# Kernel optimization log

Hardware: AMD Instinct MI355X
Metric: run time of the kernel (lower is better)

## Reference

```python
import jax, jax.numpy as jnp
import numpy as np

EPS = 1e-3          # keras BatchNormalization default epsilon
DT = 0.2
LAM2 = 4.0          # lambda_diffusion**2 = 2.0**2
K = 5

def _bn(x, gamma, beta, mean, var):
    # inference-mode batch norm over channel (last) axis
    return (x - mean) * jax.lax.rsqrt(var + EPS) * gamma + beta

def _conv(x, w):
    # NHWC 'same' conv, stride 1, no bias
    return jax.lax.conv_general_dilated(x, w, (1, 1), 'SAME',
                                        dimension_numbers=('NHWC', 'HWIO', 'NHWC'))

def _sobel_edges(x):
    # tf.image.sobel_edges: per-channel 3x3 Sobel with REFLECT padding.
    # returns (dy, dx) matching sobel[...,0], sobel[...,1]
    p = jnp.pad(x, ((0, 0), (1, 1), (1, 1), (0, 0)), mode='reflect')
    dy = (p[:, 2:, :-2] + 2 * p[:, 2:, 1:-1] + p[:, 2:, 2:]) \
       - (p[:, :-2, :-2] + 2 * p[:, :-2, 1:-1] + p[:, :-2, 2:])
    dx = (p[:, :-2, 2:] + 2 * p[:, 1:-1, 2:] + p[:, 2:, 2:]) \
       - (p[:, :-2, :-2] + 2 * p[:, 1:-1, :-2] + p[:, 2:, :-2])
    return dy, dx

def setup_inputs() -> dict:
    key = jax.random.key(0)
    k1, k2, k3 = jax.random.split(key, 3)
    B, H, W, Cin, Cout = 16, 128, 128, 64, 64
    c = jnp.float32
    return {
        'x':   jax.random.normal(k1, (B, H, W, Cin), dtype=c),
        'f_w': jax.random.normal(k2, (3, 3, Cin, Cout), dtype=c) * 0.05,
        'g_w': jax.random.normal(k3, (3, 3, Cout, Cout), dtype=c) * 0.05,
        'bnf_gamma': jnp.ones((Cin,), c),  'bnf_beta': jnp.zeros((Cin,), c),
        'bnf_mean':  jnp.zeros((Cin,), c), 'bnf_var':  jnp.ones((Cin,), c),
        'bng_gamma': jnp.ones((Cout,), c), 'bng_beta': jnp.zeros((Cout,), c),
        'bng_mean':  jnp.zeros((Cout,), c),'bng_var':  jnp.ones((Cout,), c),
        'bno_gamma': jnp.ones((Cout,), c), 'bno_beta': jnp.zeros((Cout,), c),
        'bno_mean':  jnp.zeros((Cout,), c),'bno_var':  jnp.ones((Cout,), c),
    }

def reference(x, f_w, g_w,
              bnf_gamma, bnf_beta, bnf_mean, bnf_var,
              bng_gamma, bng_beta, bng_mean, bng_var,
              bno_gamma, bno_beta, bno_mean, bno_var):
    f = _conv(jax.nn.relu(_bn(x, bnf_gamma, bnf_beta, bnf_mean, bnf_var)), f_w)
    h = f
    g = _conv(jax.nn.relu(_bn(h, bng_gamma, bng_beta, bng_mean, bng_var)), g_w)
    g1 = g
    dy, dx = _sobel_edges(h)
    Dx = 1.0 / (dy * dy / LAM2 + 1.0)   # source: sobel[..., 0]
    Dy = 1.0 / (dx * dx / LAM2 + 1.0)   # source: sobel[..., 1]
    # NOTE: faithful to source — rolls on axis=2 (W) and axis=3 (channels in NHWC)
    ux = 0.5 * (jnp.roll(g, 1, axis=2) - jnp.roll(g, -1, axis=2))
    vy = 0.5 * (jnp.roll(g1, 1, axis=3) - jnp.roll(g1, -1, axis=3))
    Ax = g * DT
    Ay = g1 * DT
    Bx = Dx * DT
    By = Dy * DT
    E = (ux + vy) * DT
    D = 1.0 / (1.0 + 2 * Bx + 2 * By)
    h0 = h
    for _ in range(K):
        prev = h
        h = D * ((1 - 2 * Bx - 2 * By) * h0
                 - 2 * E * h
                 + (-Ax + 2 * Bx) * jnp.roll(h, 1, axis=2)
                 + ( Ax + 2 * Bx) * jnp.roll(h, -1, axis=2)
                 + (-Ay + 2 * By) * jnp.roll(h, 1, axis=3)
                 + ( Ay + 2 * By) * jnp.roll(h, -1, axis=3)
                 + 2 * DT * f)
        h0 = prev
    h = jax.nn.relu(_bn(h, bno_gamma, bno_beta, bno_mean, bno_var))
    return (h, g)
```

## Files before the change

### kernel.cpp

```cpp
#include <hip/hip_runtime.h>

#define HH 128
#define WW 128
#define CC 64
#define ROW (WW*CC)
#define SLOTB 128
#define ROWB (130*SLOTB)
#define FSTR 68

typedef _Float16 half8 __attribute__((ext_vector_type(8)));
typedef _Float16 half4v __attribute__((ext_vector_type(4)));
typedef float floatx4 __attribute__((ext_vector_type(4)));

__device__ inline floatx4 rcp4(floatx4 v)
{
    floatx4 r;
    r[0] = __builtin_amdgcn_rcpf(v[0]);
    r[1] = __builtin_amdgcn_rcpf(v[1]);
    r[2] = __builtin_amdgcn_rcpf(v[2]);
    r[3] = __builtin_amdgcn_rcpf(v[3]);
    return r;
}

__global__ __launch_bounds__(256)
void repack_w(const float* __restrict__ wf, const float* __restrict__ wg,
              _Float16* __restrict__ W2f, _Float16* __restrict__ W2g)
{
    int idx = blockIdx.x * 256 + threadIdx.x;
    int sel = idx >= 36864;
    int id  = sel ? idx - 36864 : idx;
    const float* src = sel ? wg : wf;
    _Float16* dst = sel ? W2g : W2f;
    int t = id >> 12, c = (id >> 6) & 63, o = id & 63;
    int kc = c >> 5, q = (c >> 3) & 3, j = c & 7;
    int pos = ((((t*2 + kc)*4 + q)*64 + o) << 3) + j;
    dst[pos] = (_Float16)src[id];
}

template<int BNIN, int EPI>
__global__ __launch_bounds__(256, 2)
void conv_mfma(const void* __restrict__ srcv, const _Float16* __restrict__ W2,
               _Float16* __restrict__ outH, float* __restrict__ outF,
               _Float16* __restrict__ y2,
               const float* __restrict__ ig, const float* __restrict__ ib,
               const float* __restrict__ imu, const float* __restrict__ iva,
               const float* __restrict__ og, const float* __restrict__ ob,
               const float* __restrict__ om, const float* __restrict__ ov)
{
    __shared__ __align__(16) char smem[69632];
    const int t = threadIdx.x;
    const int blk = ((blockIdx.x & 7) << 7) | (blockIdx.x >> 3);
    const int b = blk >> 6, i0 = (blk & 63) * 2;

    const int c8 = (t & 7) << 3;
    float scv[8], biv[8];
    if (BNIN) {
        #pragma unroll
        for (int j = 0; j < 8; ++j) {
            float s = ig[c8+j] * rsqrtf(iva[c8+j] + 1e-3f);
            scv[j] = s; biv[j] = ib[c8+j] - imu[c8+j]*s;
        }
    }

    {
        int rr = t >> 6, s = (t >> 5) & 1;
        *(float*)(smem + rr*ROWB + (s ? 129*SLOTB : 0) + ((t & 31) << 2)) = 0.f;
    }

    if (BNIN) {
        for (int r = 0; r < 4; ++r) {
            int iy = i0 - 1 + r;
            bool inb = (iy >= 0) && (iy < HH);
            #pragma unroll
            for (int k = 0; k < 4; ++k) {
                int idx = t + (k << 8);
                int px = idx >> 3;
                half8 v = {0,0,0,0,0,0,0,0};
                if (inb) {
                    const float* gp = (const float*)srcv
                        + ((size_t)(b*HH + iy))*ROW + px*CC + c8;
                    float4 u0 = *(const float4*)gp;
                    float4 u1 = *(const float4*)(gp + 4);
                    v[0] = (_Float16)fmaxf(0.f, u0.x*scv[0] + biv[0]);
                    v[1] = (_Float16)fmaxf(0.f, u0.y*scv[1] + biv[1]);
                    v[2] = (_Float16)fmaxf(0.f, u0.z*scv[2] + biv[2]);
                    v[3] = (_Float16)fmaxf(0.f, u0.w*scv[3] + biv[3]);
                    v[4] = (_Float16)fmaxf(0.f, u1.x*scv[4] + biv[4]);
                    v[5] = (_Float16)fmaxf(0.f, u1.y*scv[5] + biv[5]);
                    v[6] = (_Float16)fmaxf(0.f, u1.z*scv[6] + biv[6]);
                    v[7] = (_Float16)fmaxf(0.f, u1.w*scv[7] + biv[7]);
                }
                int key = ((px + 1) & 7) << 4;
                *(half8*)(smem + r*ROWB + (px + 1)*SLOTB
                          + ((((t & 7) << 4)) ^ key)) = v;
            }
        }
    } else {
        const _Float16* src = (const _Float16*)srcv;
        #pragma unroll
        for (int r = 0; r < 4; ++r) {
            int iy = i0 - 1 + r;
            char* lb = smem + r*ROWB + SLOTB;
            if (iy >= 0 && iy < HH) {
                const _Float16* gp = src + (size_t)(b*HH + iy)*ROW;
                #pragma unroll
                for (int k = 0; k < 4; ++k) {
                    int eo = ((k << 8) + t) << 3;
                    __builtin_amdgcn_global_load_lds(
                        (const __attribute__((address_space(1))) void*)(gp + eo),
                        (__attribute__((address_space(3))) void*)(lb + (eo << 1)),
                        16, 0, 0);
                }
            } else {
                half8 z = {0,0,0,0,0,0,0,0};
                #pragma unroll
                for (int k = 0; k < 4; ++k)
                    *(half8*)(lb + (((k << 8) + t) << 4)) = z;
            }
        }
    }
    __syncthreads();

    const int wv = t >> 6, lane = t & 63;
    const int lm = lane & 15, quad = lane >> 4;
    const int r  = wv >> 1;
    const int px0 = (wv & 1) * 64;
    floatx4 z4 = {0.f,0.f,0.f,0.f};
    floatx4 acc[4][4];
    #pragma unroll
    for (int ms = 0; ms < 4; ++ms)
        #pragma unroll
        for (int nt = 0; nt < 4; ++nt) acc[ms][nt] = z4;

    #pragma unroll
    for (int tap = 0; tap < 9; ++tap) {
        const int di = tap / 3, dj = tap % 3;
        const int slot = px0 + lm + dj;
        const int key  = (slot & 7) << 4;
        const char* abase = smem + (r + di)*ROWB + slot*SLOTB;
        #pragma unroll
        for (int kc = 0; kc < 2; ++kc) {
            const char* ab = abase + ((kc*64 + quad*16) ^ key);
            half8 a0 = *(const half8*)(ab);
            half8 a1 = *(const half8*)(ab + 16*SLOTB);
            half8 a2 = *(const half8*)(ab + 32*SLOTB);
            half8 a3 = *(const half8*)(ab + 48*SLOTB);
            const _Float16* wb = W2 + (((tap*2 + kc)*4 + quad) << 9) + (lm << 3);
            half8 b0 = *(const half8*)(wb);
            half8 b1 = *(const half8*)(wb + 128);
            half8 b2 = *(const half8*)(wb + 256);
            half8 b3 = *(const half8*)(wb + 384);
            acc[0][0] = __builtin_amdgcn_mfma_f32_16x16x32_f16(a0, b0, acc[0][0], 0,0,0);
            acc[1][0] = __builtin_amdgcn_mfma_f32_16x16x32_f16(a1, b0, acc[1][0], 0,0,0);
            acc[2][0] = __builtin_amdgcn_mfma_f32_16x16x32_f16(a2, b0, acc[2][0], 0,0,0);
            acc[3][0] = __builtin_amdgcn_mfma_f32_16x16x32_f16(a3, b0, acc[3][0], 0,0,0);
            acc[0][1] = __builtin_amdgcn_mfma_f32_16x16x32_f16(a0, b1, acc[0][1], 0,0,0);
            acc[1][1] = __builtin_amdgcn_mfma_f32_16x16x32_f16(a1, b1, acc[1][1], 0,0,0);
            acc[2][1] = __builtin_amdgcn_mfma_f32_16x16x32_f16(a2, b1, acc[2][1], 0,0,0);
            acc[3][1] = __builtin_amdgcn_mfma_f32_16x16x32_f16(a3, b1, acc[3][1], 0,0,0);
            acc[0][2] = __builtin_amdgcn_mfma_f32_16x16x32_f16(a0, b2, acc[0][2], 0,0,0);
            acc[1][2] = __builtin_amdgcn_mfma_f32_16x16x32_f16(a1, b2, acc[1][2], 0,0,0);
            acc[2][2] = __builtin_amdgcn_mfma_f32_16x16x32_f16(a2, b2, acc[2][2], 0,0,0);
            acc[3][2] = __builtin_amdgcn_mfma_f32_16x16x32_f16(a3, b2, acc[3][2], 0,0,0);
            acc[0][3] = __builtin_amdgcn_mfma_f32_16x16x32_f16(a0, b3, acc[0][3], 0,0,0);
            acc[1][3] = __builtin_amdgcn_mfma_f32_16x16x32_f16(a1, b3, acc[1][3], 0,0,0);
            acc[2][3] = __builtin_amdgcn_mfma_f32_16x16x32_f16(a2, b3, acc[2][3], 0,0,0);
            acc[3][3] = __builtin_amdgcn_mfma_f32_16x16x32_f16(a3, b3, acc[3][3], 0,0,0);
        }
    }

    __syncthreads();
    float* sF = (float*)smem;
    #pragma unroll
    for (int nt = 0; nt < 4; ++nt) {
        int c = nt*16 + lm;
        #pragma unroll
        for (int ms = 0; ms < 4; ++ms) {
            int pix = r*128 + px0 + ms*16 + quad*4;
            floatx4 v = acc[ms][nt];
            #pragma unroll
            for (int rv = 0; rv < 4; ++rv)
                sF[(pix + rv)*FSTR + c] = v[rv];
        }
    }
    __syncthreads();

    const size_t gbase = ((size_t)(b*HH + i0)) * ROW;
    if (EPI) {
        const int c8o = (t & 7) << 3;
        float s8[8], bb8[8];
        #pragma unroll
        for (int j = 0; j < 8; ++j) {
            float ss = og[c8o+j] * rsqrtf(ov[c8o+j] + 1e-3f);
            s8[j] = ss; bb8[j] = ob[c8o+j] - om[c8o+j]*ss;
        }
        #pragma unroll
        for (int jj = 0; jj < 8; ++jj) {
            int chunk = jj*256 + t;
            int px = chunk >> 3;
            const float* sp = sF + px*FSTR + c8o;
            floatx4 u0 = *(const floatx4*)(sp);
            floatx4 u1 = *(const floatx4*)(sp + 4);
            half8 hv, yv;
            #pragma unroll
            for (int j = 0; j < 4; ++j) {
                hv[j]   = (_Float16)u0[j];
                hv[4+j] = (_Float16)u1[j];
                yv[j]   = (_Float16)fmaxf(0.f, u0[j]*s8[j]   + bb8[j]);
                yv[4+j] = (_Float16)fmaxf(0.f, u1[j]*s8[4+j] + bb8[4+j]);
            }
            size_t oe = gbase + (size_t)px*64 + c8o;
            *(half8*)(outH + oe) = hv;
            int key8 = ((px + 1) & 7) << 3;
            *(half8*)(y2 + gbase + (size_t)px*64 + (c8o ^ key8)) = yv;
        }
    } else {
        #pragma unroll
        for (int jj = 0; jj < 8; ++jj) {
            int chunk = jj*256 + t;
            int px = chunk >> 3;
            const int cc = (t & 7) << 3;
            const float* sp = sF + px*FSTR + cc;
            size_t oe = gbase + (size_t)px*64 + cc;
            *(floatx4*)(outF + oe)     = *(const floatx4*)(sp);
            *(floatx4*)(outF + oe + 4) = *(const floatx4*)(sp + 4);
        }
    }
}

__global__ __launch_bounds__(1024, 2)
void diffuse(const _Float16* __restrict__ f, const float* __restrict__ g,
             float* __restrict__ out,
             const float* __restrict__ bog, const float* __restrict__ bob,
             const float* __restrict__ bom, const float* __restrict__ bov)
{
    __shared__ float B0[ROW], B1[ROW];
    const int t = threadIdx.x;
    const int rowb = ((blockIdx.x & 7) << 8) | (blockIdx.x >> 3);
    const int b = rowb >> 7, i = rowb & 127;
    const int im = (i == 0)    ? 1    : i - 1;
    const int ip = (i == HH-1) ? HH-2 : i + 1;
    const _Float16* fb  = f + (size_t)b * (HH*ROW);
    const _Float16* frm = fb + (size_t)im * ROW;
    const _Float16* fr0 = fb + (size_t)i  * ROW;
    const _Float16* frp = fb + (size_t)ip * ROW;
    const float* grow = g + (size_t)rowb * ROW;

    const int lane = t & 63;
    const int srcm = (lane & 48) | ((lane - 1) & 15);
    const int srcp = (lane & 48) | ((lane + 1) & 15);
    const int w0 = t >> 4, c0 = (t & 15) << 2;
    const int qch[2] = { t*4, t*4 + 4096 };
    const int wch[2] = { w0, w0 + 64 };

    #pragma unroll
    for (int k = 0; k < 2; ++k) {
        half4v vm = *(const half4v*)(frm + qch[k]);
        half4v vp = *(const half4v*)(frp + qch[k]);
        floatx4 a = { (float)vm[0], (float)vm[1], (float)vm[2], (float)vm[3] };
        floatx4 p = { (float)vp[0], (float)vp[1], (float)vp[2], (float)vp[3] };
        *(floatx4*)(B0 + qch[k]) = a;
        *(floatx4*)(B1 + qch[k]) = p;
    }
    __syncthreads();

    floatx4 Bx4[2], dxp4[2];
    #pragma unroll
    for (int k = 0; k < 2; ++k) {
        int w = wch[k];
        int wm = (w == 0)    ? 1      : w - 1;
        int wp = (w == WW-1) ? WW - 2 : w + 1;
        floatx4 am = *(const floatx4*)(B0 + wm*CC + c0);
        floatx4 a0 = *(const floatx4*)(B0 + w *CC + c0);
        floatx4 ap = *(const floatx4*)(B0 + wp*CC + c0);
        floatx4 bm = *(const floatx4*)(B1 + wm*CC + c0);
        floatx4 b0 = *(const floatx4*)(B1 + w *CC + c0);
        floatx4 bp = *(const floatx4*)(B1 + wp*CC + c0);
        floatx4 dy = (bm + 2.f*b0 + bp) - (am + 2.f*a0 + ap);
        Bx4[k]  = 0.2f * rcp4(dy*dy*0.25f + 1.f);
        dxp4[k] = (ap - am) + (bp - bm);
    }
    __syncthreads();

    #pragma unroll
    for (int k = 0; k < 2; ++k) {
        half4v v0 = *(const half4v*)(fr0 + qch[k]);
        floatx4 fv = { (float)v0[0], (float)v0[1], (float)v0[2], (float)v0[3] };
        *(floatx4*)(B0 + qch[k]) = fv;
        *(floatx4*)(B1 + qch[k]) = *(const floatx4*)(grow + qch[k]);
    }
    __syncthreads();

    floatx4 cR4[2], cL4[2], cU4[2], cH0[2], cEE[2], cF[2], h4[2], h04[2];
    #pragma unroll
    for (int k = 0; k < 2; ++k) {
        int w = wch[k];
        int wm = (w == 0)    ? 1      : w - 1;
        int wp = (w == WW-1) ? WW - 2 : w + 1;
        int wl = (w + WW - 1) & (WW - 1);
        int wr = (w + 1) & (WW - 1);
        floatx4 fm = *(const floatx4*)(B0 + wm*CC + c0);
        floatx4 fv = *(const floatx4*)(B0 + w *CC + c0);
        floatx4 fp = *(const floatx4*)(B0 + wp*CC + c0);
        floatx4 dx = dxp4[k] + 2.f*(fp - fm);
        floatx4 By = 0.2f * rcp4(dx*dx*0.25f + 1.f);
        floatx4 Bx = Bx4[k];
        floatx4 gv = *(const floatx4*)(B1 + w *CC + c0);
        floatx4 gl = *(const floatx4*)(B1 + wl*CC + c0);
        floatx4 gr = *(const floatx4*)(B1 + wr*CC + c0);
        float gdm = __shfl(gv[3], srcm, 64);
        float gup = __shfl(gv[0], srcp, 64);
        floatx4 gd = { gdm, gv[0], gv[1], gv[2] };
        floatx4 gu = { gv[1], gv[2], gv[3], gup };
        floatx4 E  = ((gl - gr) + (gd - gu)) * 0.1f;
        floatx4 Dd = rcp4(1.f + 2.f*Bx + 2.f*By);
        floatx4 P  = 2.f * Bx * Dd;
        floatx4 R  = 2.f * By * Dd;
        floatx4 Q  = (gv * 0.2f) * Dd;
        cR4[k] = P + Q;
        cL4[k] = P - Q;
        cU4[k] = R + Q;
        cH0[k] = 2.f*Dd - 1.f;
        cEE[k] = -2.f * E * Dd;
        cF[k]  = 0.4f * Dd * fv;
        h4[k] = fv; h04[k] = fv;
    }
    __syncthreads();

    int oWl[2], oWr[2];
    #pragma unroll
    for (int k = 0; k < 2; ++k) {
        int w = wch[k];
        oWl[k] = ((w + WW - 1) & (WW - 1))*CC + c0;
        oWr[k] = ((w + 1) & (WW - 1))*CC + c0;
    }

    float* cur = B0;
    float* oth = B1;
    for (int it = 0; it < 5; ++it) {
        #pragma unroll
        for (int k = 0; k < 2; ++k) {
            floatx4 hl = *(const floatx4*)(cur + oWl[k]);
            floatx4 hr = *(const floatx4*)(cur + oWr[k]);
            floatx4 hv = h4[k];
            float hdm = __shfl(hv[3], srcm, 64);
            float hup = __shfl(hv[0], srcp, 64);
            floatx4 hd = { hdm, hv[0], hv[1], hv[2] };
            floatx4 hu = { hv[1], hv[2], hv[3], hup };
            floatx4 cD = (cU4[k] - cR4[k]) + cL4[k];
            floatx4 hn = cH0[k]*h04[k] + cEE[k]*hv
                       + cR4[k]*hr + cL4[k]*hl
                       + cU4[k]*hu + cD*hd + cF[k];
            if (it < 4)
                *(floatx4*)(oth + qch[k]) = hn;
            h04[k] = hv; h4[k] = hn;
        }
        if (it < 4) {
            __syncthreads();
            float* tmp = cur; cur = oth; oth = tmp;
        }
    }

    floatx4 gg = *(const floatx4*)(bog + c0);
    floatx4 vv = *(const floatx4*)(bov + c0);
    floatx4 bb = *(const floatx4*)(bob + c0);
    floatx4 mm = *(const floatx4*)(bom + c0);
    floatx4 s4, bi4;
    #pragma unroll
    for (int j = 0; j < 4; ++j) s4[j] = gg[j] * rsqrtf(vv[j] + 1e-3f);
    bi4 = bb - mm*s4;
    float* op = out + (size_t)rowb * ROW;
    #pragma unroll
    for (int k = 0; k < 2; ++k) {
        floatx4 rr = h4[k]*s4 + bi4;
        #pragma unroll
        for (int j = 0; j < 4; ++j) rr[j] = fmaxf(0.f, rr[j]);
        *(floatx4*)(op + qch[k]) = rr;
    }
}

extern "C" void kernel_launch(void* const* d_in, const int* in_sizes, int n_in,
                              void* d_out, int out_size, void* d_ws, size_t ws_size,
                              hipStream_t stream)
{
    const float* x    = (const float*)d_in[0];
    const float* f_w  = (const float*)d_in[1];
    const float* g_w  = (const float*)d_in[2];
    const float* bnf_g = (const float*)d_in[3];
    const float* bnf_b = (const float*)d_in[4];
    const float* bnf_m = (const float*)d_in[5];
    const float* bnf_v = (const float*)d_in[6];
    const float* bng_g = (const float*)d_in[7];
    const float* bng_b = (const float*)d_in[8];
    const float* bng_m = (const float*)d_in[9];
    const float* bng_v = (const float*)d_in[10];
    const float* bno_g = (const float*)d_in[11];
    const float* bno_b = (const float*)d_in[12];
    const float* bno_m = (const float*)d_in[13];
    const float* bno_v = (const float*)d_in[14];

    float* out = (float*)d_out;
    const size_t N = (size_t)16 * HH * WW * CC;
    _Float16* y2   = (_Float16*)d_ws;
    _Float16* fbuf = y2 + N;
    _Float16* W2f  = y2 + 2*N;
    _Float16* W2g  = W2f + 36864;

    repack_w<<<288, 256, 0, stream>>>(f_w, g_w, W2f, W2g);
    conv_mfma<1,1><<<1024, 256, 0, stream>>>(x, W2f, fbuf, nullptr, y2,
                                             bnf_g, bnf_b, bnf_m, bnf_v,
                                             bng_g, bng_b, bng_m, bng_v);
    conv_mfma<0,0><<<1024, 256, 0, stream>>>(y2, W2g, nullptr, out + N, nullptr,
                                             nullptr, nullptr, nullptr, nullptr,
                                             nullptr, nullptr, nullptr, nullptr);
    diffuse<<<2048, 1024, 0, stream>>>(fbuf, out + N, out, bno_g, bno_b, bno_m, bno_v);
}
```

Baseline: 321.1 us.

## Stream eight output rows per conv block through a six-row LDS ring

The two convolution kernels now give each block eight consecutive output rows instead of two, using a 256-block grid. Input rows sit in a six-slot LDS ring. The next two rows are prefetched while the MFMA loop runs, by async global-to-LDS DMA or by register staging for the BN-fused path. This cuts the halo re-reads of input rows and overlaps loads with compute. In exchange each CU runs only one 4-wave block, and each row pair pays extra barriers for the epilogue.

```diff
diff --git a/kernel.cpp b/kernel.cpp
--- a/kernel.cpp
+++ b/kernel.cpp
@@ -6,6 +6,8 @@
 #define ROW (WW*CC)
 #define SLOTB 128
 #define ROWB (130*SLOTB)
+#define NRING 6
+#define RINGB (NRING*ROWB)
 #define FSTR 68
 
 typedef _Float16 half8 __attribute__((ext_vector_type(8)));
@@ -38,192 +40,250 @@
 }
 
 template<int BNIN, int EPI>
-__global__ __launch_bounds__(256, 2)
-void conv_mfma(const void* __restrict__ srcv, const _Float16* __restrict__ W2,
-               _Float16* __restrict__ outH, float* __restrict__ outF,
-               _Float16* __restrict__ y2,
-               const float* __restrict__ ig, const float* __restrict__ ib,
-               const float* __restrict__ imu, const float* __restrict__ iva,
-               const float* __restrict__ og, const float* __restrict__ ob,
-               const float* __restrict__ om, const float* __restrict__ ov)
+__global__ __launch_bounds__(256)
+void conv_stream(const void* __restrict__ srcv, const _Float16* __restrict__ W2,
+                 _Float16* __restrict__ outH, float* __restrict__ outF,
+                 _Float16* __restrict__ y2,
+                 const float* __restrict__ ig, const float* __restrict__ ib,
+                 const float* __restrict__ imu, const float* __restrict__ iva,
+                 const float* __restrict__ og, const float* __restrict__ ob,
+                 const float* __restrict__ om, const float* __restrict__ ov)
 {
-    __shared__ __align__(16) char smem[69632];
+    __shared__ __align__(16) char smem[RINGB + 128*FSTR*4];
     const int t = threadIdx.x;
-    const int blk = ((blockIdx.x & 7) << 7) | (blockIdx.x >> 3);
-    const int b = blk >> 6, i0 = (blk & 63) * 2;
+    const int swz = ((blockIdx.x & 7) << 5) | (blockIdx.x >> 3);
+    const int b = swz >> 4, s = swz & 15;
+    const int r0 = s << 3;
 
     const int c8 = (t & 7) << 3;
     float scv[8], biv[8];
     if (BNIN) {
         #pragma unroll
         for (int j = 0; j < 8; ++j) {
-            float s = ig[c8+j] * rsqrtf(iva[c8+j] + 1e-3f);
-            scv[j] = s; biv[j] = ib[c8+j] - imu[c8+j]*s;
-        }
-    }
-
-    {
-        int rr = t >> 6, s = (t >> 5) & 1;
-        *(float*)(smem + rr*ROWB + (s ? 129*SLOTB : 0) + ((t & 31) << 2)) = 0.f;
-    }
-
-    if (BNIN) {
-        for (int r = 0; r < 4; ++r) {
-            int iy = i0 - 1 + r;
-            bool inb = (iy >= 0) && (iy < HH);
+            float sc = ig[c8+j] * rsqrtf(iva[c8+j] + 1e-3f);
+            scv[j] = sc; biv[j] = ib[c8+j] - imu[c8+j]*sc;
+        }
+    }
+    float s8o[8], bb8o[8];
+    if (EPI) {
+        #pragma unroll
+        for (int j = 0; j < 8; ++j) {
+            float ss = og[c8+j] * rsqrtf(ov[c8+j] + 1e-3f);
+            s8o[j] = ss; bb8o[j] = ob[c8+j] - om[c8+j]*ss;
+        }
+    }
+
+    for (int k = t; k < 384; k += 256) {
+        int rs = k >> 6, e = (k >> 5) & 1, dw = k & 31;
+        *(float*)(smem + rs*ROWB + (e ? 129*SLOTB : 0) + (dw << 2)) = 0.f;
+    }
+
+    auto stage_dma = [&](int l) {
+        int iy = r0 - 1 + l;
+        int slot = (l >= NRING) ? l - NRING : l;
+        char* lb = smem + slot*ROWB + SLOTB;
+        if (iy >= 0 && iy < HH) {
+            const _Float16* gp = (const _Float16*)srcv + (size_t)(b*HH + iy)*ROW;
             #pragma unroll
             for (int k = 0; k < 4; ++k) {
-                int idx = t + (k << 8);
-                int px = idx >> 3;
-                half8 v = {0,0,0,0,0,0,0,0};
-                if (inb) {
-                    const float* gp = (const float*)srcv
-                        + ((size_t)(b*HH + iy))*ROW + px*CC + c8;
-                    float4 u0 = *(const float4*)gp;
-                    float4 u1 = *(const float4*)(gp + 4);
-                    v[0] = (_Float16)fmaxf(0.f, u0.x*scv[0] + biv[0]);
-                    v[1] = (_Float16)fmaxf(0.f, u0.y*scv[1] + biv[1]);
-                    v[2] = (_Float16)fmaxf(0.f, u0.z*scv[2] + biv[2]);
-                    v[3] = (_Float16)fmaxf(0.f, u0.w*scv[3] + biv[3]);
-                    v[4] = (_Float16)fmaxf(0.f, u1.x*scv[4] + biv[4]);
-                    v[5] = (_Float16)fmaxf(0.f, u1.y*scv[5] + biv[5]);
-                    v[6] = (_Float16)fmaxf(0.f, u1.z*scv[6] + biv[6]);
-                    v[7] = (_Float16)fmaxf(0.f, u1.w*scv[7] + biv[7]);
-                }
-                int key = ((px + 1) & 7) << 4;
-                *(half8*)(smem + r*ROWB + (px + 1)*SLOTB
-                          + ((((t & 7) << 4)) ^ key)) = v;
-            }
-        }
-    } else {
-        const _Float16* src = (const _Float16*)srcv;
-        #pragma unroll
-        for (int r = 0; r < 4; ++r) {
-            int iy = i0 - 1 + r;
-            char* lb = smem + r*ROWB + SLOTB;
+                int eo = ((k << 8) + t) << 3;
+                __builtin_amdgcn_global_load_lds(
+                    (const __attribute__((address_space(1))) void*)(gp + eo),
+                    (__attribute__((address_space(3))) void*)(lb + (eo << 1)),
+                    16, 0, 0);
+            }
+        } else {
+            half8 z = {};
+            #pragma unroll
+            for (int k = 0; k < 4; ++k)
+                *(half8*)(lb + (((k << 8) + t) << 4)) = z;
+        }
+    };
+    auto stage_bn_now = [&](int l) {
+        int iy = r0 - 1 + l;
+        int slot = (l >= NRING) ? l - NRING : l;
+        char* sb = smem + slot*ROWB;
+        #pragma unroll
+        for (int k = 0; k < 4; ++k) {
+            int px = (((k << 8) + t) >> 3);
+            half8 v = {};
             if (iy >= 0 && iy < HH) {
-                const _Float16* gp = src + (size_t)(b*HH + iy)*ROW;
-                #pragma unroll
-                for (int k = 0; k < 4; ++k) {
-                    int eo = ((k << 8) + t) << 3;
-                    __builtin_amdgcn_global_load_lds(
-                        (const __attribute__((address_space(1))) void*)(gp + eo),
-                        (__attribute__((address_space(3))) void*)(lb + (eo << 1)),
-                        16, 0, 0);
-                }
-            } else {
-                half8 z = {0,0,0,0,0,0,0,0};
-                #pragma unroll
-                for (int k = 0; k < 4; ++k)
-                    *(half8*)(lb + (((k << 8) + t) << 4)) = z;
-            }
-        }
-    }
+                const float* gp = (const float*)srcv
+                    + (size_t)(b*HH + iy)*ROW + px*CC + c8;
+                float4 u0 = *(const float4*)gp;
+                float4 u1 = *(const float4*)(gp + 4);
+                v[0] = (_Float16)fmaxf(0.f, u0.x*scv[0] + biv[0]);
+                v[1] = (_Float16)fmaxf(0.f, u0.y*scv[1] + biv[1]);
+                v[2] = (_Float16)fmaxf(0.f, u0.z*scv[2] + biv[2]);
+                v[3] = (_Float16)fmaxf(0.f, u0.w*scv[3] + biv[3]);
+                v[4] = (_Float16)fmaxf(0.f, u1.x*scv[4] + biv[4]);
+                v[5] = (_Float16)fmaxf(0.f, u1.y*scv[5] + biv[5]);
+                v[6] = (_Float16)fmaxf(0.f, u1.z*scv[6] + biv[6]);
+                v[7] = (_Float16)fmaxf(0.f, u1.w*scv[7] + biv[7]);
+            }
+            *(half8*)(sb + (px + 1)*SLOTB
+                      + (((t & 7) << 4) ^ (((px + 1) & 7) << 4))) = v;
+        }
+    };
+
+    if (BNIN) { stage_bn_now(0); stage_bn_now(1); stage_bn_now(2); stage_bn_now(3); }
+    else      { stage_dma(0);    stage_dma(1);    stage_dma(2);    stage_dma(3);    }
     __syncthreads();
 
     const int wv = t >> 6, lane = t & 63;
     const int lm = lane & 15, quad = lane >> 4;
     const int r  = wv >> 1;
     const int px0 = (wv & 1) * 64;
-    floatx4 z4 = {0.f,0.f,0.f,0.f};
-    floatx4 acc[4][4];
-    #pragma unroll
-    for (int ms = 0; ms < 4; ++ms)
-        #pragma unroll
-        for (int nt = 0; nt < 4; ++nt) acc[ms][nt] = z4;
-
-    #pragma unroll
-    for (int tap = 0; tap < 9; ++tap) {
-        const int di = tap / 3, dj = tap % 3;
-        const int slot = px0 + lm + dj;
-        const int key  = (slot & 7) << 4;
-        const char* abase = smem + (r + di)*ROWB + slot*SLOTB;
-        #pragma unroll
-        for (int kc = 0; kc < 2; ++kc) {
-            const char* ab = abase + ((kc*64 + quad*16) ^ key);
-            half8 a0 = *(const half8*)(ab);
-            half8 a1 = *(const half8*)(ab + 16*SLOTB);
-            half8 a2 = *(const half8*)(ab + 32*SLOTB);
-            half8 a3 = *(const half8*)(ab + 48*SLOTB);
-            const _Float16* wb = W2 + (((tap*2 + kc)*4 + quad) << 9) + (lm << 3);
-            half8 b0 = *(const half8*)(wb);
-            half8 b1 = *(const half8*)(wb + 128);
-            half8 b2 = *(const half8*)(wb + 256);
-            half8 b3 = *(const half8*)(wb + 384);
-            acc[0][0] = __builtin_amdgcn_mfma_f32_16x16x32_f16(a0, b0, acc[0][0], 0,0,0);
-            acc[1][0] = __builtin_amdgcn_mfma_f32_16x16x32_f16(a1, b0, acc[1][0], 0,0,0);
-            acc[2][0] = __builtin_amdgcn_mfma_f32_16x16x32_f16(a2, b0, acc[2][0], 0,0,0);
-            acc[3][0] = __builtin_amdgcn_mfma_f32_16x16x32_f16(a3, b0, acc[3][0], 0,0,0);
-            acc[0][1] = __builtin_amdgcn_mfma_f32_16x16x32_f16(a0, b1, acc[0][1], 0,0,0);
-            acc[1][1] = __builtin_amdgcn_mfma_f32_16x16x32_f16(a1, b1, acc[1][1], 0,0,0);
-            acc[2][1] = __builtin_amdgcn_mfma_f32_16x16x32_f16(a2, b1, acc[2][1], 0,0,0);
-            acc[3][1] = __builtin_amdgcn_mfma_f32_16x16x32_f16(a3, b1, acc[3][1], 0,0,0);
-            acc[0][2] = __builtin_amdgcn_mfma_f32_16x16x32_f16(a0, b2, acc[0][2], 0,0,0);
-            acc[1][2] = __builtin_amdgcn_mfma_f32_16x16x32_f16(a1, b2, acc[1][2], 0,0,0);
-            acc[2][2] = __builtin_amdgcn_mfma_f32_16x16x32_f16(a2, b2, acc[2][2], 0,0,0);
-            acc[3][2] = __builtin_amdgcn_mfma_f32_16x16x32_f16(a3, b2, acc[3][2], 0,0,0);
-            acc[0][3] = __builtin_amdgcn_mfma_f32_16x16x32_f16(a0, b3, acc[0][3], 0,0,0);
-            acc[1][3] = __builtin_amdgcn_mfma_f32_16x16x32_f16(a1, b3, acc[1][3], 0,0,0);
-            acc[2][3] = __builtin_amdgcn_mfma_f32_16x16x32_f16(a2, b3, acc[2][3], 0,0,0);
-            acc[3][3] = __builtin_amdgcn_mfma_f32_16x16x32_f16(a3, b3, acc[3][3], 0,0,0);
-        }
-    }
-
-    __syncthreads();
-    float* sF = (float*)smem;
-    #pragma unroll
-    for (int nt = 0; nt < 4; ++nt) {
-        int c = nt*16 + lm;
-        #pragma unroll
-        for (int ms = 0; ms < 4; ++ms) {
-            int pix = r*128 + px0 + ms*16 + quad*4;
-            floatx4 v = acc[ms][nt];
+    float* sF = (float*)(smem + RINGB);
+
+    #pragma unroll 1
+    for (int p = 0; p < 4; ++p) {
+        float4 stg[2][4][2];
+        int sv[2] = {0, 0};
+        if (p < 3) {
+            if (BNIN) {
+                #pragma unroll
+                for (int q = 0; q < 2; ++q) {
+                    int iy = r0 - 1 + (2*p + 4 + q);
+                    sv[q] = (iy >= 0) && (iy < HH);
+                    if (sv[q]) {
+                        const float* gr = (const float*)srcv
+                            + (size_t)(b*HH + iy)*ROW + c8;
+                        #pragma unroll
+                        for (int k = 0; k < 4; ++k) {
+                            int px = (((k << 8) + t) >> 3);
+                            stg[q][k][0] = *(const float4*)(gr + px*CC);
+                            stg[q][k][1] = *(const float4*)(gr + px*CC + 4);
+                        }
+                    }
+                }
+            } else {
+                stage_dma(2*p + 4);
+                stage_dma(2*p + 5);
+            }
+        }
+
+        floatx4 z4 = {0.f,0.f,0.f,0.f};
+        floatx4 acc[4][4];
+        #pragma unroll
+        for (int ms = 0; ms < 4; ++ms)
             #pragma unroll
-            for (int rv = 0; rv < 4; ++rv)
-                sF[(pix + rv)*FSTR + c] = v[rv];
-        }
-    }
-    __syncthreads();
-
-    const size_t gbase = ((size_t)(b*HH + i0)) * ROW;
-    if (EPI) {
-        const int c8o = (t & 7) << 3;
-        float s8[8], bb8[8];
-        #pragma unroll
-        for (int j = 0; j < 8; ++j) {
-            float ss = og[c8o+j] * rsqrtf(ov[c8o+j] + 1e-3f);
-            s8[j] = ss; bb8[j] = ob[c8o+j] - om[c8o+j]*ss;
-        }
-        #pragma unroll
-        for (int jj = 0; jj < 8; ++jj) {
-            int chunk = jj*256 + t;
-            int px = chunk >> 3;
-            const float* sp = sF + px*FSTR + c8o;
-            floatx4 u0 = *(const floatx4*)(sp);
-            floatx4 u1 = *(const floatx4*)(sp + 4);
-            half8 hv, yv;
+            for (int nt = 0; nt < 4; ++nt) acc[ms][nt] = z4;
+
+        const int l0 = 2*p + r;
+        #pragma unroll
+        for (int tap = 0; tap < 9; ++tap) {
+            const int di = tap / 3, dj = tap % 3;
+            int rs = l0 + di; if (rs >= NRING) rs -= NRING;
+            const int slot = px0 + lm + dj;
+            const int key  = (slot & 7) << 4;
+            const char* abase = smem + rs*ROWB + slot*SLOTB;
             #pragma unroll
-            for (int j = 0; j < 4; ++j) {
-                hv[j]   = (_Float16)u0[j];
-                hv[4+j] = (_Float16)u1[j];
-                yv[j]   = (_Float16)fmaxf(0.f, u0[j]*s8[j]   + bb8[j]);
-                yv[4+j] = (_Float16)fmaxf(0.f, u1[j]*s8[4+j] + bb8[4+j]);
-            }
-            size_t oe = gbase + (size_t)px*64 + c8o;
-            *(half8*)(outH + oe) = hv;
-            int key8 = ((px + 1) & 7) << 3;
-            *(half8*)(y2 + gbase + (size_t)px*64 + (c8o ^ key8)) = yv;
-        }
-    } else {
-        #pragma unroll
-        for (int jj = 0; jj < 8; ++jj) {
-            int chunk = jj*256 + t;
-            int px = chunk >> 3;
-            const int cc = (t & 7) << 3;
-            const float* sp = sF + px*FSTR + cc;
-            size_t oe = gbase + (size_t)px*64 + cc;
-            *(floatx4*)(outF + oe)     = *(const floatx4*)(sp);
-            *(floatx4*)(outF + oe + 4) = *(const floatx4*)(sp + 4);
+            for (int kc = 0; kc < 2; ++kc) {
+                const char* ab = abase + ((kc*64 + quad*16) ^ key);
+                half8 a0 = *(const half8*)(ab);
+                half8 a1 = *(const half8*)(ab + 16*SLOTB);
+                half8 a2 = *(const half8*)(ab + 32*SLOTB);
+                half8 a3 = *(const half8*)(ab + 48*SLOTB);
+                const _Float16* wb = W2 + (((tap*2 + kc)*4 + quad) << 9) + (lm << 3);
+                half8 b0 = *(const half8*)(wb);
+                half8 b1 = *(const half8*)(wb + 128);
+                half8 b2 = *(const half8*)(wb + 256);
+                half8 b3 = *(const half8*)(wb + 384);
+                acc[0][0] = __builtin_amdgcn_mfma_f32_16x16x32_f16(a0, b0, acc[0][0], 0,0,0);
+                acc[1][0] = __builtin_amdgcn_mfma_f32_16x16x32_f16(a1, b0, acc[1][0], 0,0,0);
+                acc[2][0] = __builtin_amdgcn_mfma_f32_16x16x32_f16(a2, b0, acc[2][0], 0,0,0);
+                acc[3][0] = __builtin_amdgcn_mfma_f32_16x16x32_f16(a3, b0, acc[3][0], 0,0,0);
+                acc[0][1] = __builtin_amdgcn_mfma_f32_16x16x32_f16(a0, b1, acc[0][1], 0,0,0);
+                acc[1][1] = __builtin_amdgcn_mfma_f32_16x16x32_f16(a1, b1, acc[1][1], 0,0,0);
+                acc[2][1] = __builtin_amdgcn_mfma_f32_16x16x32_f16(a2, b1, acc[2][1], 0,0,0);
+                acc[3][1] = __builtin_amdgcn_mfma_f32_16x16x32_f16(a3, b1, acc[3][1], 0,0,0);
+                acc[0][2] = __builtin_amdgcn_mfma_f32_16x16x32_f16(a0, b2, acc[0][2], 0,0,0);
+                acc[1][2] = __builtin_amdgcn_mfma_f32_16x16x32_f16(a1, b2, acc[1][2], 0,0,0);
+                acc[2][2] = __builtin_amdgcn_mfma_f32_16x16x32_f16(a2, b2, acc[2][2], 0,0,0);
+                acc[3][2] = __builtin_amdgcn_mfma_f32_16x16x32_f16(a3, b2, acc[3][2], 0,0,0);
+                acc[0][3] = __builtin_amdgcn_mfma_f32_16x16x32_f16(a0, b3, acc[0][3], 0,0,0);
+                acc[1][3] = __builtin_amdgcn_mfma_f32_16x16x32_f16(a1, b3, acc[1][3], 0,0,0);
+                acc[2][3] = __builtin_amdgcn_mfma_f32_16x16x32_f16(a2, b3, acc[2][3], 0,0,0);
+                acc[3][3] = __builtin_amdgcn_mfma_f32_16x16x32_f16(a3, b3, acc[3][3], 0,0,0);
+            }
+        }
+
+        if (BNIN && p < 3) {
+            #pragma unroll
+            for (int q = 0; q < 2; ++q) {
+                int l = 2*p + 4 + q;
+                int slot = (l >= NRING) ? l - NRING : l;
+                char* sb = smem + slot*ROWB;
+                #pragma unroll
+                for (int k = 0; k < 4; ++k) {
+                    int px = (((k << 8) + t) >> 3);
+                    half8 v = {};
+                    if (sv[q]) {
+                        float4 u0 = stg[q][k][0], u1 = stg[q][k][1];
+                        v[0] = (_Float16)fmaxf(0.f, u0.x*scv[0] + biv[0]);
+                        v[1] = (_Float16)fmaxf(0.f, u0.y*scv[1] + biv[1]);
+                        v[2] = (_Float16)fmaxf(0.f, u0.z*scv[2] + biv[2]);
+                        v[3] = (_Float16)fmaxf(0.f, u0.w*scv[3] + biv[3]);
+                        v[4] = (_Float16)fmaxf(0.f, u1.x*scv[4] + biv[4]);
+                        v[5] = (_Float16)fmaxf(0.f, u1.y*scv[5] + biv[5]);
+                        v[6] = (_Float16)fmaxf(0.f, u1.z*scv[6] + biv[6]);
+                        v[7] = (_Float16)fmaxf(0.f, u1.w*scv[7] + biv[7]);
+                    }
+                    *(half8*)(sb + (px + 1)*SLOTB
+                              + (((t & 7) << 4) ^ (((px + 1) & 7) << 4))) = v;
+                }
+            }
+        }
+
+        #pragma unroll
+        for (int rr = 0; rr < 2; ++rr) {
+            if ((wv >> 1) == rr) {
+                #pragma unroll
+                for (int nt = 0; nt < 4; ++nt) {
+                    int c = nt*16 + lm;
+                    #pragma unroll
+                    for (int ms = 0; ms < 4; ++ms) {
+                        int pix = px0 + ms*16 + quad*4;
+                        floatx4 v = acc[ms][nt];
+                        #pragma unroll
+                        for (int rv = 0; rv < 4; ++rv)
+                            sF[(pix + rv)*FSTR + c] = v[rv];
+                    }
+                }
+            }
+            __syncthreads();
+            const size_t gb = ((size_t)(b*HH + r0 + 2*p + rr)) * ROW;
+            if (EPI) {
+                #pragma unroll
+                for (int k = 0; k < 4; ++k) {
+                    int px = (((k << 8) + t) >> 3);
+                    const float* sp = sF + px*FSTR + c8;
+                    floatx4 u0 = *(const floatx4*)(sp);
+                    floatx4 u1 = *(const floatx4*)(sp + 4);
+                    half8 hv, yv;
+                    #pragma unroll
+                    for (int j = 0; j < 4; ++j) {
+                        hv[j]   = (_Float16)u0[j];
+                        hv[4+j] = (_Float16)u1[j];
+                        yv[j]   = (_Float16)fmaxf(0.f, u0[j]*s8o[j]   + bb8o[j]);
+                        yv[4+j] = (_Float16)fmaxf(0.f, u1[j]*s8o[4+j] + bb8o[4+j]);
+                    }
+                    *(half8*)(outH + gb + (size_t)px*CC + c8) = hv;
+                    int key8 = ((px + 1) & 7) << 3;
+                    *(half8*)(y2 + gb + (size_t)px*CC + (c8 ^ key8)) = yv;
+                }
+            } else {
+                #pragma unroll
+                for (int k = 0; k < 4; ++k) {
+                    int px = (((k << 8) + t) >> 3);
+                    const float* sp = sF + px*FSTR + c8;
+                    size_t oe = gb + (size_t)px*CC + c8;
+                    *(floatx4*)(outF + oe)     = *(const floatx4*)(sp);
+                    *(floatx4*)(outF + oe + 4) = *(const floatx4*)(sp + 4);
+                }
+            }
+            __syncthreads();
         }
     }
 }
@@ -407,11 +467,11 @@
     _Float16* W2g  = W2f + 36864;
 
     repack_w<<<288, 256, 0, stream>>>(f_w, g_w, W2f, W2g);
-    conv_mfma<1,1><<<1024, 256, 0, stream>>>(x, W2f, fbuf, nullptr, y2,
-                                             bnf_g, bnf_b, bnf_m, bnf_v,
-                                             bng_g, bng_b, bng_m, bng_v);
-    conv_mfma<0,0><<<1024, 256, 0, stream>>>(y2, W2g, nullptr, out + N, nullptr,
-                                             nullptr, nullptr, nullptr, nullptr,
-                                             nullptr, nullptr, nullptr, nullptr);
+    conv_stream<1,1><<<256, 256, 0, stream>>>(x, W2f, fbuf, nullptr, y2,
+                                              bnf_g, bnf_b, bnf_m, bnf_v,
+                                              bng_g, bng_b, bng_m, bng_v);
+    conv_stream<0,0><<<256, 256, 0, stream>>>(y2, W2g, nullptr, out + N, nullptr,
+                                              nullptr, nullptr, nullptr, nullptr,
+                                              nullptr, nullptr, nullptr, nullptr);
     diffuse<<<2048, 1024, 0, stream>>>(fbuf, out + N, out, bno_g, bno_b, bno_m, bno_v);
 }
```

Result: slower. 353.4 us (+10.1%).

## Fuse second convolution into diffusion kernel via per-row MFMA

Applied to the files above, without the earlier changes.

Removes the separate g-convolution launch and computes g for each image row inside the diffusion kernel. Three input rows of y2 are loaded into LDS with global_load_lds, and the 3x3 conv runs as MFMA. The result is written to shared memory for the stencil and also to the global g output. This removes the write and re-read of g through global memory and one launch. In exchange it adds LDS use, loads the weights redundantly in every block, and raises launch_bounds occupancy to 4, which may cause register spills.

```diff
diff --git a/kernel.cpp b/kernel.cpp
--- a/kernel.cpp
+++ b/kernel.cpp
@@ -211,7 +211,8 @@
             }
             size_t oe = gbase + (size_t)px*64 + c8o;
             *(half8*)(outH + oe) = hv;
-            int key8 = ((px + 1) & 7) << 3;
+            int pxr = px & 127;
+            int key8 = ((pxr + 1) & 7) << 3;
             *(half8*)(y2 + gbase + (size_t)px*64 + (c8o ^ key8)) = yv;
         }
     } else {
@@ -228,12 +229,14 @@
     }
 }
 
-__global__ __launch_bounds__(1024, 2)
-void diffuse(const _Float16* __restrict__ f, const float* __restrict__ g,
-             float* __restrict__ out,
-             const float* __restrict__ bog, const float* __restrict__ bob,
-             const float* __restrict__ bom, const float* __restrict__ bov)
+__global__ __launch_bounds__(1024, 4)
+void diffuse_fused(const _Float16* __restrict__ f, const _Float16* __restrict__ y2,
+                   const _Float16* __restrict__ W2g,
+                   float* __restrict__ gout, float* __restrict__ out,
+                   const float* __restrict__ bog, const float* __restrict__ bob,
+                   const float* __restrict__ bom, const float* __restrict__ bov)
 {
+    __shared__ __align__(16) char S[3*ROWB];
     __shared__ float B0[ROW], B1[ROW];
     const int t = threadIdx.x;
     const int rowb = ((blockIdx.x & 7) << 8) | (blockIdx.x >> 3);
@@ -244,7 +247,6 @@
     const _Float16* frm = fb + (size_t)im * ROW;
     const _Float16* fr0 = fb + (size_t)i  * ROW;
     const _Float16* frp = fb + (size_t)ip * ROW;
-    const float* grow = g + (size_t)rowb * ROW;
 
     const int lane = t & 63;
     const int srcm = (lane & 48) | ((lane - 1) & 15);
@@ -253,6 +255,30 @@
     const int qch[2] = { t*4, t*4 + 4096 };
     const int wch[2] = { w0, w0 + 64 };
 
+    if (t < 192) {
+        int rr = t >> 6, s = (t >> 5) & 1;
+        *(float*)(S + rr*ROWB + (s ? 129*SLOTB : 0) + ((t & 31) << 2)) = 0.f;
+    }
+    {
+        const _Float16* yb = y2 + (size_t)b * (HH*ROW);
+        #pragma unroll
+        for (int r = 0; r < 3; ++r) {
+            int iy = i - 1 + r;
+            char* lb = S + r*ROWB + SLOTB;
+            if (iy >= 0 && iy < HH) {
+                const _Float16* gp = yb + (size_t)iy*ROW + t*8;
+                __builtin_amdgcn_global_load_lds(
+                    (const __attribute__((address_space(1))) void*)gp,
+                    (__attribute__((address_space(3))) void*)(lb + t*16),
+                    16, 0, 0);
+            } else {
+                half8 z = {};
+                *(half8*)(lb + t*16) = z;
+            }
+        }
+    }
+    half4v v0a = *(const half4v*)(fr0 + qch[0]);
+    half4v v0b = *(const half4v*)(fr0 + qch[1]);
     #pragma unroll
     for (int k = 0; k < 2; ++k) {
         half4v vm = *(const half4v*)(frm + qch[k]);
@@ -280,17 +306,51 @@
         Bx4[k]  = 0.2f * rcp4(dy*dy*0.25f + 1.f);
         dxp4[k] = (ap - am) + (bp - bm);
     }
-    __syncthreads();
-
-    #pragma unroll
-    for (int k = 0; k < 2; ++k) {
-        half4v v0 = *(const half4v*)(fr0 + qch[k]);
-        floatx4 fv = { (float)v0[0], (float)v0[1], (float)v0[2], (float)v0[3] };
-        *(floatx4*)(B0 + qch[k]) = fv;
-        *(floatx4*)(B1 + qch[k]) = *(const floatx4*)(grow + qch[k]);
-    }
-    __syncthreads();
-
+
+    const int wv = t >> 6;
+    const int lm = lane & 15, quad = lane >> 4;
+    const int px0 = (wv & 7) << 4, chh = wv >> 3;
+    floatx4 ga0 = {0.f,0.f,0.f,0.f}, ga1 = {0.f,0.f,0.f,0.f};
+    #pragma unroll
+    for (int tap = 0; tap < 9; ++tap) {
+        const int di = tap / 3, dj = tap % 3;
+        const int slot = px0 + lm + dj;
+        const int key  = (slot & 7) << 4;
+        const char* abase = S + di*ROWB + slot*SLOTB;
+        #pragma unroll
+        for (int kc = 0; kc < 2; ++kc) {
+            const char* ab = abase + ((kc*64 + quad*16) ^ key);
+            half8 a0 = *(const half8*)(ab);
+            const _Float16* wb = W2g + (((tap*2 + kc)*4 + quad) << 9)
+                               + (chh << 8) + (lm << 3);
+            half8 b0 = *(const half8*)(wb);
+            half8 b1 = *(const half8*)(wb + 128);
+            ga0 = __builtin_amdgcn_mfma_f32_16x16x32_f16(a0, b0, ga0, 0,0,0);
+            ga1 = __builtin_amdgcn_mfma_f32_16x16x32_f16(a0, b1, ga1, 0,0,0);
+        }
+    }
+    __syncthreads();
+
+    {
+        floatx4 f0 = { (float)v0a[0], (float)v0a[1], (float)v0a[2], (float)v0a[3] };
+        floatx4 f1 = { (float)v0b[0], (float)v0b[1], (float)v0b[2], (float)v0b[3] };
+        *(floatx4*)(B0 + qch[0]) = f0;
+        *(floatx4*)(B0 + qch[1]) = f1;
+    }
+    {
+        int cbase = chh*32 + lm;
+        #pragma unroll
+        for (int nt = 0; nt < 2; ++nt) {
+            floatx4 v = nt ? ga1 : ga0;
+            int c = cbase + nt*16;
+            #pragma unroll
+            for (int rv = 0; rv < 4; ++rv)
+                B1[(px0 + quad*4 + rv)*CC + c] = v[rv];
+        }
+    }
+    __syncthreads();
+
+    float* gop = gout + (size_t)rowb * ROW;
     floatx4 cR4[2], cL4[2], cU4[2], cH0[2], cEE[2], cF[2], h4[2], h04[2];
     #pragma unroll
     for (int k = 0; k < 2; ++k) {
@@ -308,6 +368,7 @@
         floatx4 gv = *(const floatx4*)(B1 + w *CC + c0);
         floatx4 gl = *(const floatx4*)(B1 + wl*CC + c0);
         floatx4 gr = *(const floatx4*)(B1 + wr*CC + c0);
+        *(floatx4*)(gop + qch[k]) = gv;
         float gdm = __shfl(gv[3], srcm, 64);
         float gup = __shfl(gv[0], srcp, 64);
         floatx4 gd = { gdm, gv[0], gv[1], gv[2] };
@@ -410,8 +471,6 @@
     conv_mfma<1,1><<<1024, 256, 0, stream>>>(x, W2f, fbuf, nullptr, y2,
                                              bnf_g, bnf_b, bnf_m, bnf_v,
                                              bng_g, bng_b, bng_m, bng_v);
-    conv_mfma<0,0><<<1024, 256, 0, stream>>>(y2, W2g, nullptr, out + N, nullptr,
-                                             nullptr, nullptr, nullptr, nullptr,
-                                             nullptr, nullptr, nullptr, nullptr);
-    diffuse<<<2048, 1024, 0, stream>>>(fbuf, out + N, out, bno_g, bno_b, bno_m, bno_v);
+    diffuse_fused<<<2048, 1024, 0, stream>>>(fbuf, y2, W2g, out + N, out,
+                                             bno_g, bno_b, bno_m, bno_v);
 }
```

After: 336.4 us. 1.05x slower.
